# Kernel tuning notes

Hardware: AMD Instinct MI355X
Metric: run time of the kernel (lower is better)

The kernel has to match this reference:

```python
import jax, jax.numpy as jnp
import numpy as np
from jax import lax

B, S, H, T = 64, 512, 1024, 21


def setup_inputs() -> dict:
    key = jax.random.key(0)
    k1, k2, k3, k4, k5, k6, k7 = jax.random.split(key, 7)
    hidden_states = jax.random.normal(k1, (B, S, H), dtype=jnp.float32)
    attention_mask = jnp.ones((B, S), dtype=jnp.int32)
    labels = jax.random.randint(k2, (B, S), 0, T).astype(jnp.int64)
    W = jax.random.normal(k3, (T, H), dtype=jnp.float32) * 0.02
    b = jnp.zeros((T,), dtype=jnp.float32)
    # torchcrf init: uniform(-0.1, 0.1)
    transitions = jax.random.uniform(k4, (T, T), minval=-0.1, maxval=0.1, dtype=jnp.float32)
    start_transitions = jax.random.uniform(k5, (T,), minval=-0.1, maxval=0.1, dtype=jnp.float32)
    end_transitions = jax.random.uniform(k6, (T,), minval=-0.1, maxval=0.1, dtype=jnp.float32)
    return {
        "hidden_states": hidden_states,
        "attention_mask": attention_mask,
        "labels": labels,
        "W": W,
        "b": b,
        "transitions": transitions,
        "start_transitions": start_transitions,
        "end_transitions": end_transitions,
    }


def _crf_log_likelihood(emissions, labels, mask, trans, start, end):
    # emissions [B,S,T], labels [B,S] int, mask [B,S] bool. reduction='sum'.
    Bn, Sn, Tn = emissions.shape
    maskf = mask.astype(emissions.dtype)
    emit_scores = jnp.take_along_axis(emissions, labels[:, :, None], axis=2)[:, :, 0]  # [B,S]
    trans_scores = trans[labels[:, :-1], labels[:, 1:]]  # [B,S-1]
    numerator = start[labels[:, 0]] + emit_scores[:, 0]
    numerator = numerator + jnp.sum((trans_scores + emit_scores[:, 1:]) * maskf[:, 1:], axis=1)
    seq_ends = jnp.sum(mask.astype(jnp.int32), axis=1) - 1  # [B]
    last_tags = labels[jnp.arange(Bn), seq_ends]
    numerator = numerator + end[last_tags]
    # partition via forward algorithm (scan over time)
    alpha0 = start[None, :] + emissions[:, 0]  # [B,T]
    def step(alpha, inp):
        emit_t, mask_t = inp  # [B,T], [B]
        nxt = jax.nn.logsumexp(alpha[:, :, None] + trans[None, :, :] + emit_t[:, None, :], axis=1)
        return jnp.where(mask_t[:, None], nxt, alpha), None
    alpha, _ = lax.scan(step, alpha0, (emissions[:, 1:].transpose(1, 0, 2), mask[:, 1:].T))
    log_Z = jax.nn.logsumexp(alpha + end[None, :], axis=1)  # [B]
    return jnp.sum(numerator - log_Z)


def _viterbi_decode(emissions, mask, trans, start, end):
    Bn, Sn, Tn = emissions.shape
    score0 = start[None, :] + emissions[:, 0]  # [B,T]
    identity_bp = jnp.broadcast_to(jnp.arange(Tn)[None, :], (Bn, Tn))
    def fwd(score, inp):
        emit_t, mask_t = inp
        broad = score[:, :, None] + trans[None, :, :]  # [B, prev, cur]
        best_prev = jnp.argmax(broad, axis=1)  # [B,T]
        nxt = jnp.max(broad, axis=1) + emit_t
        new_score = jnp.where(mask_t[:, None], nxt, score)
        bp = jnp.where(mask_t[:, None], best_prev, identity_bp)
        return new_score, bp
    final_score, bps = lax.scan(fwd, score0, (emissions[:, 1:].transpose(1, 0, 2), mask[:, 1:].T))
    last_tag = jnp.argmax(final_score + end[None, :], axis=1)  # [B] tag at pos S-1
    def back(tag, bp_t):
        prev = jnp.take_along_axis(bp_t, tag[:, None], axis=1)[:, 0]
        return prev, tag
    tag0, tags_rest = lax.scan(back, last_tag, bps, reverse=True)  # tags_rest[t] = tag at pos t+1
    tags = jnp.concatenate([tag0[None, :], tags_rest], axis=0).T  # [B,S]
    return jnp.where(mask, tags, 0).astype(jnp.int64)


def reference(hidden_states, attention_mask, labels, W, b, transitions, start_transitions, end_transitions):
    mask = attention_mask.astype(bool)
    # dropout is identity in eval mode
    emissions = jnp.einsum("bsh,th->bst", hidden_states, W) + b  # [B,S,T]
    log_prob = _crf_log_likelihood(emissions, labels, mask, transitions, start_transitions, end_transitions)
    loss = -log_prob
    pred = _viterbi_decode(emissions, mask, transitions, start_transitions, end_transitions)
    return loss, pred
```

## Files before the change

kernel.cpp:

```cpp
#include <hip/hip_runtime.h>
#include <math.h>
#include <stdint.h>

#define BB 64
#define SS 512
#define HH 1024
#define TT 21

template <int CTRL>
__device__ __forceinline__ float dpp_add(float v) {
  int t = __builtin_amdgcn_update_dpp(0, __float_as_int(v), CTRL, 0xF, 0xF, true);
  return v + __int_as_float(t);
}
__device__ __forceinline__ float wave_sum(float v) {
  v = dpp_add<0x121>(v);
  v = dpp_add<0x122>(v);
  v = dpp_add<0x124>(v);
  v = dpp_add<0x128>(v);
  v += __shfl_xor(v, 16);
  v += __shfl_xor(v, 32);
  return v;
}

#define DOT4(A, H, WV)    \
  A = fmaf(H.x, WV.x, A); \
  A = fmaf(H.y, WV.y, A); \
  A = fmaf(H.z, WV.z, A); \
  A = fmaf(H.w, WV.w, A)

__global__ __launch_bounds__(192, 4) void k_emis(const float* __restrict__ hs,
                                                 const float* __restrict__ W,
                                                 const float* __restrict__ bias,
                                                 float* __restrict__ emis) {
  __shared__ float part[192 * 14];
  const int tid = threadIdx.x;
  const int q = tid & 7;
  const int tmp = tid >> 3;
  const int tg = tmp % 3;
  const int rp = tmp / 3;
  const size_t row0 = (size_t)blockIdx.x * 16 + rp * 2;
  const float4* hp0 = (const float4*)(hs + row0 * HH);
  const float4* hp1 = (const float4*)(hs + (row0 + 1) * HH);
  const float* wb0 = W + (size_t)(tg * 7) * HH + q * 4;

  float a0[7] = {0.f, 0.f, 0.f, 0.f, 0.f, 0.f, 0.f};
  float a1[7] = {0.f, 0.f, 0.f, 0.f, 0.f, 0.f, 0.f};
  float4 h0 = hp0[q], h1 = hp1[q];
#pragma unroll 2
  for (int i = 0; i < 32; ++i) {
    const float4 hc0 = h0, hc1 = h1;
    if (i < 31) {
      h0 = hp0[(i + 1) * 8 + q];
      h1 = hp1[(i + 1) * 8 + q];
    }
    const float* wb = wb0 + (size_t)i * 32;
#pragma unroll
    for (int lt = 0; lt < 7; ++lt) {
      const float4 w = *(const float4*)(wb + (size_t)lt * HH);
      DOT4(a0[lt], hc0, w);
      DOT4(a1[lt], hc1, w);
    }
  }
#pragma unroll
  for (int lt = 0; lt < 7; ++lt) {
    part[tid * 14 + lt] = a0[lt];
    part[tid * 14 + 7 + lt] = a1[lt];
  }
  __syncthreads();

  for (int o = tid; o < 16 * TT; o += 192) {
    const int rr = o / TT;
    const int t = o - rr * TT;
    const int tg2 = t / 7;
    const int lt2 = t - tg2 * 7;
    const float* pp = part + (((rr >> 1) * 3 + tg2) * 8) * 14 + (rr & 1) * 7 + lt2;
    float s = ((pp[0] + pp[14]) + (pp[28] + pp[42])) +
              ((pp[56] + pp[70]) + (pp[84] + pp[98]));
    emis[(size_t)blockIdx.x * (16 * TT) + o] = s + bias[t];
  }
}

#define RLF(V, K) __int_as_float(__builtin_amdgcn_readlane(__float_as_int(V), K))

__global__ __launch_bounds__(64, 1) void k_scan2(const float* __restrict__ emis,
                                                 const int* __restrict__ mask,
                                                 const int* __restrict__ labels,
                                                 const float* __restrict__ trans,
                                                 const float* __restrict__ sv,
                                                 const float* __restrict__ ev,
                                                 float* __restrict__ outv,
                                                 float* __restrict__ pred,
                                                 unsigned* __restrict__ done) {
  __shared__ float sE[SS * TT];
  __shared__ unsigned long long mb[9];
  __shared__ unsigned char bp[SS][32];
  __shared__ unsigned char sTag[SS];
  const int lane = threadIdx.x;

  if (blockIdx.x >= 128) {
    float a = 1.0001f, b2 = 0.9999f, c = 0.5f, d = 1.5f;
    for (int it = 0; it < 2048; ++it) {
#pragma unroll 128
      for (int k = 0; k < 128; ++k) {
        a = fmaf(a, 1.000001f, 1e-7f);
        b2 = fmaf(b2, 0.999999f, 2e-7f);
        c = fmaf(c, 1.000002f, 3e-7f);
        d = fmaf(d, 0.999998f, 4e-7f);
      }
      if (__hip_atomic_load(done, __ATOMIC_RELAXED, __HIP_MEMORY_SCOPE_AGENT) >= 128u)
        break;
    }
    asm volatile("" ::"v"(a), "v"(b2), "v"(c), "v"(d));
    return;
  }

  const int j = lane;
  const bool act = (j < TT);
  const int jj = act ? j : 0;
  const int b = blockIdx.x & 63;

  {
    const float4* src = (const float4*)(emis + (size_t)b * SS * TT);
    float4* dst = (float4*)sE;
    for (int i = lane; i < SS * TT / 4; i += 64) dst[i] = src[i];
#pragma unroll
    for (int w = 0; w < 8; ++w) {
      unsigned long long bm = __ballot(mask[b * SS + w * 64 + lane] != 0);
      if (lane == 0) mb[w] = bm;
    }
    if (lane == 0) mb[8] = 0ull;
  }
  __syncthreads();

  if (blockIdx.x < 64) {
    float E[TT];
#pragma unroll
    for (int i = 0; i < TT; ++i) E[i] = __expf(trans[i * TT + jj]);
    float v = act ? __expf(sv[jj] + sE[jj]) : 0.f;
    float C = 0.f;
    float nxtv[8];
#pragma unroll
    for (int k = 0; k < 8; ++k) nxtv[k] = sE[(1 + k) * TT + jj];

#define CRF_STEP(P, SHB)                                                      \
  {                                                                           \
    const int mk = (int)((swin >> ((SHB) + (P))) & 1ull);                     \
    const float ge_t = ge[P];                                                 \
    const float v0 = RLF(v, 0), v1 = RLF(v, 1), v2 = RLF(v, 2);               \
    const float v3 = RLF(v, 3), v4 = RLF(v, 4), v5 = RLF(v, 5);               \
    const float v6 = RLF(v, 6), v7 = RLF(v, 7), v8 = RLF(v, 8);               \
    const float v9 = RLF(v, 9), v10 = RLF(v, 10), v11 = RLF(v, 11);           \
    const float v12 = RLF(v, 12), v13 = RLF(v, 13), v14 = RLF(v, 14);         \
    const float v15 = RLF(v, 15), v16 = RLF(v, 16), v17 = RLF(v, 17);         \
    const float v18 = RLF(v, 18), v19 = RLF(v, 19), v20 = RLF(v, 20);         \
    float scale = 1.0f;                                                       \
    if ((P) == 7) {                                                           \
      float m = fmaxf(fmaxf(fmaxf(v0, v1), fmaxf(v2, v3)),                    \
                      fmaxf(fmaxf(v4, v5), fmaxf(v6, v7)));                   \
      m = fmaxf(m, fmaxf(fmaxf(v8, v9), fmaxf(v10, v11)));                    \
      m = fmaxf(m, fmaxf(fmaxf(v12, v13), fmaxf(v14, v15)));                  \
      m = fmaxf(m, fmaxf(fmaxf(v16, v17), fmaxf(v18, v19)));                  \
      m = fmaxf(m, v20);                                                      \
      int ex = (int)((__float_as_uint(m) >> 23) & 255u) - 127;                \
      scale = __uint_as_float((unsigned)(127 - ex) << 23);                    \
      C += (float)ex * 0.6931471805599453f;                                   \
      v *= scale;                                                             \
    }                                                                         \
    float q0 = v0 * E[0], q1 = v1 * E[1], q2 = v2 * E[2];                     \
    q0 = fmaf(v3, E[3], q0);   q1 = fmaf(v4, E[4], q1);   q2 = fmaf(v5, E[5], q2);   \
    q0 = fmaf(v6, E[6], q0);   q1 = fmaf(v7, E[7], q1);   q2 = fmaf(v8, E[8], q2);   \
    q0 = fmaf(v9, E[9], q0);   q1 = fmaf(v10, E[10], q1); q2 = fmaf(v11, E[11], q2); \
    q0 = fmaf(v12, E[12], q0); q1 = fmaf(v13, E[13], q1); q2 = fmaf(v14, E[14], q2); \
    q0 = fmaf(v15, E[15], q0); q1 = fmaf(v16, E[16], q1); q2 = fmaf(v17, E[17], q2); \
    q0 = fmaf(v18, E[18], q0); q1 = fmaf(v19, E[19], q1); q2 = fmaf(v20, E[20], q2); \
    float vn = ((q0 + q1 + q2) * scale) * ge_t;                               \
    v = (act && mk) ? vn : v;                                                 \
  }

#pragma unroll 1
    for (int w = 0; w < 8; ++w) {
      const unsigned long long wa = mb[w], wb2 = mb[w + 1];
      const unsigned long long winv = (wa >> 1) | (wb2 << 63);
      const unsigned wlo = __builtin_amdgcn_readfirstlane((unsigned)winv);
      const unsigned whi = __builtin_amdgcn_readfirstlane((unsigned)(winv >> 32));
      const unsigned long long swin = ((unsigned long long)whi << 32) | wlo;
      const int nci = (w < 7) ? 8 : 7;
#pragma unroll 1
      for (int ci = 0; ci < nci; ++ci) {
        const int t0 = ((w << 3) + ci) * 8 + 1;
        float cur[8], ge[8];
#pragma unroll
        for (int k = 0; k < 8; ++k) cur[k] = nxtv[k];
#pragma unroll
        for (int k = 0; k < 8; ++k) ge[k] = __expf(cur[k]);
#pragma unroll
        for (int k = 0; k < 8; ++k) {
          int tl = t0 + 8 + k;
          tl = (tl < SS) ? tl : (SS - 1);
          nxtv[k] = sE[tl * TT + jj];
        }
        const int shb = ci << 3;
#pragma unroll
        for (int p = 0; p < 8; ++p) { CRF_STEP(p, shb); }
      }
      if (w == 7) {
        float cur[8], ge[8];
#pragma unroll
        for (int k = 0; k < 7; ++k) cur[k] = nxtv[k];
#pragma unroll
        for (int k = 0; k < 7; ++k) ge[k] = __expf(cur[k]);
#pragma unroll
        for (int p = 0; p < 7; ++p) { CRF_STEP(p, 56); }
      }
    }
#undef CRF_STEP
    float wv = act ? v * __expf(ev[jj]) : 0.f;
#pragma unroll
    for (int d = 32; d >= 1; d >>= 1) wv += __shfl_xor(wv, d);
    const float logZv = C + __logf(wv);

    int cnt = 0;
#pragma unroll
    for (int w = 0; w < 8; ++w) cnt += (int)__popcll(mb[w]);
    const int* lab = labels + b * SS;
    float p = 0.f;
    for (int t = lane; t < SS; t += 64) {
      if (t >= 1) {
        const int lp = lab[t - 1];
        const int lc = lab[t];
        const float mk = (float)((mb[t >> 6] >> (t & 63)) & 1ull);
        p += mk * (trans[lp * TT + lc] + sE[t * TT + lc]);
      }
    }
    p = wave_sum(p);
    if (lane == 0) {
      const int l0 = lab[0];
      float numer = p + sv[l0] + sE[l0];
      numer += ev[lab[cnt - 1]];
      atomicAdd(outv, logZv - numer);
      atomicAdd(done, 1u);
    }
  } else {
    float Tc[TT];
#pragma unroll
    for (int i = 0; i < TT; ++i) Tc[i] = trans[i * TT + jj];
    float sc = act ? (sv[jj] + sE[jj]) : -3.0e38f;
    float nxtv[8];
#pragma unroll
    for (int k = 0; k < 8; ++k) nxtv[k] = sE[(1 + k) * TT + jj];

#define ARGSTEP(BV, BI, VAL, IDX)          \
  {                                        \
    float x_ = (VAL) + Tc[IDX];            \
    if (x_ > BV) { BV = x_; BI = (IDX); }  \
  }
#define VIT_STEP(P, SHB, TCUR)                                                \
  {                                                                           \
    const int mk = (int)((swin >> ((SHB) + (P))) & 1ull);                     \
    const float e = cur[P];                                                   \
    const float s0 = RLF(sc, 0), s1 = RLF(sc, 1), s2 = RLF(sc, 2);            \
    const float s3 = RLF(sc, 3), s4 = RLF(sc, 4), s5 = RLF(sc, 5);            \
    const float s6 = RLF(sc, 6), s7 = RLF(sc, 7), s8 = RLF(sc, 8);            \
    const float s9 = RLF(sc, 9), s10 = RLF(sc, 10), s11 = RLF(sc, 11);        \
    const float s12 = RLF(sc, 12), s13 = RLF(sc, 13), s14 = RLF(sc, 14);      \
    const float s15 = RLF(sc, 15), s16 = RLF(sc, 16), s17 = RLF(sc, 17);      \
    const float s18 = RLF(sc, 18), s19 = RLF(sc, 19), s20 = RLF(sc, 20);      \
    float b0v, b1v, b2v;                                                      \
    int i0, i1, i2;                                                           \
    b0v = s0 + Tc[0]; i0 = 0;                                                 \
    b1v = s1 + Tc[1]; i1 = 1;                                                 \
    b2v = s2 + Tc[2]; i2 = 2;                                                 \
    ARGSTEP(b0v, i0, s3, 3);   ARGSTEP(b1v, i1, s4, 4);   ARGSTEP(b2v, i2, s5, 5);    \
    ARGSTEP(b0v, i0, s6, 6);   ARGSTEP(b1v, i1, s7, 7);   ARGSTEP(b2v, i2, s8, 8);    \
    ARGSTEP(b0v, i0, s9, 9);   ARGSTEP(b1v, i1, s10, 10); ARGSTEP(b2v, i2, s11, 11);  \
    ARGSTEP(b0v, i0, s12, 12); ARGSTEP(b1v, i1, s13, 13); ARGSTEP(b2v, i2, s14, 14);  \
    ARGSTEP(b0v, i0, s15, 15); ARGSTEP(b1v, i1, s16, 16); ARGSTEP(b2v, i2, s17, 17);  \
    ARGSTEP(b0v, i0, s18, 18); ARGSTEP(b1v, i1, s19, 19); ARGSTEP(b2v, i2, s20, 20);  \
    float best = b0v;                                                         \
    int bi = i0;                                                              \
    if (b1v > best || (b1v == best && i1 < bi)) { best = b1v; bi = i1; }      \
    if (b2v > best || (b2v == best && i2 < bi)) { best = b2v; bi = i2; }      \
    float ns = best + e;                                                      \
    sc = (act && mk) ? ns : sc;                                               \
    if (act) bp[TCUR][j] = (unsigned char)(mk ? bi : j);                      \
  }

#pragma unroll 1
    for (int w = 0; w < 8; ++w) {
      const unsigned long long wa = mb[w], wb2 = mb[w + 1];
      const unsigned long long winv = (wa >> 1) | (wb2 << 63);
      const unsigned wlo = __builtin_amdgcn_readfirstlane((unsigned)winv);
      const unsigned whi = __builtin_amdgcn_readfirstlane((unsigned)(winv >> 32));
      const unsigned long long swin = ((unsigned long long)whi << 32) | wlo;
      const int nci = (w < 7) ? 8 : 7;
#pragma unroll 1
      for (int ci = 0; ci < nci; ++ci) {
        const int t0 = ((w << 3) + ci) * 8 + 1;
        float cur[8];
#pragma unroll
        for (int k = 0; k < 8; ++k) cur[k] = nxtv[k];
#pragma unroll
        for (int k = 0; k < 8; ++k) {
          int tl = t0 + 8 + k;
          tl = (tl < SS) ? tl : (SS - 1);
          nxtv[k] = sE[tl * TT + jj];
        }
        const int shb = ci << 3;
#pragma unroll
        for (int p = 0; p < 8; ++p) { VIT_STEP(p, shb, t0 + p); }
      }
      if (w == 7) {
        float cur[8];
#pragma unroll
        for (int k = 0; k < 7; ++k) cur[k] = nxtv[k];
#pragma unroll
        for (int p = 0; p < 7; ++p) { VIT_STEP(p, 56, 505 + p); }
      }
    }
#undef VIT_STEP
#undef ARGSTEP
    float fsv = act ? (sc + ev[jj]) : -3.0e38f;
    int idx = j;
#pragma unroll
    for (int d = 32; d >= 1; d >>= 1) {
      float ov = __shfl_xor(fsv, d);
      int oi = __shfl_xor(idx, d);
      bool take = (ov > fsv) || (ov == fsv && oi < idx);
      fsv = take ? ov : fsv;
      idx = take ? oi : idx;
    }
    __syncthreads();
    if (lane == 0) {
      int tag = idx;
      sTag[SS - 1] = (unsigned char)tag;
      for (int t = SS - 1; t >= 1; --t) {
        tag = bp[t][tag];
        sTag[t - 1] = (unsigned char)tag;
      }
    }
    __syncthreads();
    for (int i = lane; i < SS; i += 64) {
      pred[(size_t)b * SS + i] = (float)(mask[b * SS + i] ? (int)sTag[i] : 0);
    }
    if (lane == 0) atomicAdd(done, 1u);
  }
}

extern "C" void kernel_launch(void* const* d_in, const int* in_sizes, int n_in,
                              void* d_out, int out_size, void* d_ws, size_t ws_size,
                              hipStream_t stream) {
  const float* hs = (const float*)d_in[0];
  const int* msk = (const int*)d_in[1];
  const int* lab = (const int*)d_in[2];
  const float* W = (const float*)d_in[3];
  const float* bias = (const float*)d_in[4];
  const float* trans = (const float*)d_in[5];
  const float* sv = (const float*)d_in[6];
  const float* ev = (const float*)d_in[7];
  float* out = (float*)d_out;

  float* emis = (float*)d_ws;
  unsigned* done = (unsigned*)((char*)d_ws + (size_t)BB * SS * TT * 4);

  hipMemsetAsync(d_out, 0, 4, stream);
  hipMemsetAsync(done, 0, 4, stream);
  k_emis<<<2048, 192, 0, stream>>>(hs, W, bias, emis);
  k_scan2<<<512, 64, 0, stream>>>(emis, msk, lab, trans, sv, ev, out, out + 1, done);
}
```

Measured before the change: 450.5 us.

## Fuse emission GEMM into per-batch CRF/Viterbi block with pipelined producer waves

Result: slower. 1.792 ms (+297.7%).

```diff
diff --git a/kernel.cpp b/kernel.cpp
--- a/kernel.cpp
+++ b/kernel.cpp
@@ -28,131 +28,53 @@
   A = fmaf(H.z, WV.z, A); \
   A = fmaf(H.w, WV.w, A)
 
-__global__ __launch_bounds__(192, 4) void k_emis(const float* __restrict__ hs,
-                                                 const float* __restrict__ W,
-                                                 const float* __restrict__ bias,
-                                                 float* __restrict__ emis) {
-  __shared__ float part[192 * 14];
-  const int tid = threadIdx.x;
-  const int q = tid & 7;
-  const int tmp = tid >> 3;
-  const int tg = tmp % 3;
-  const int rp = tmp / 3;
-  const size_t row0 = (size_t)blockIdx.x * 16 + rp * 2;
-  const float4* hp0 = (const float4*)(hs + row0 * HH);
-  const float4* hp1 = (const float4*)(hs + (row0 + 1) * HH);
-  const float* wb0 = W + (size_t)(tg * 7) * HH + q * 4;
-
-  float a0[7] = {0.f, 0.f, 0.f, 0.f, 0.f, 0.f, 0.f};
-  float a1[7] = {0.f, 0.f, 0.f, 0.f, 0.f, 0.f, 0.f};
-  float4 h0 = hp0[q], h1 = hp1[q];
-#pragma unroll 2
-  for (int i = 0; i < 32; ++i) {
-    const float4 hc0 = h0, hc1 = h1;
-    if (i < 31) {
-      h0 = hp0[(i + 1) * 8 + q];
-      h1 = hp1[(i + 1) * 8 + q];
-    }
-    const float* wb = wb0 + (size_t)i * 32;
-#pragma unroll
-    for (int lt = 0; lt < 7; ++lt) {
-      const float4 w = *(const float4*)(wb + (size_t)lt * HH);
-      DOT4(a0[lt], hc0, w);
-      DOT4(a1[lt], hc1, w);
-    }
-  }
-#pragma unroll
-  for (int lt = 0; lt < 7; ++lt) {
-    part[tid * 14 + lt] = a0[lt];
-    part[tid * 14 + 7 + lt] = a1[lt];
-  }
-  __syncthreads();
-
-  for (int o = tid; o < 16 * TT; o += 192) {
-    const int rr = o / TT;
-    const int t = o - rr * TT;
-    const int tg2 = t / 7;
-    const int lt2 = t - tg2 * 7;
-    const float* pp = part + (((rr >> 1) * 3 + tg2) * 8) * 14 + (rr & 1) * 7 + lt2;
-    float s = ((pp[0] + pp[14]) + (pp[28] + pp[42])) +
-              ((pp[56] + pp[70]) + (pp[84] + pp[98]));
-    emis[(size_t)blockIdx.x * (16 * TT) + o] = s + bias[t];
-  }
-}
-
 #define RLF(V, K) __int_as_float(__builtin_amdgcn_readlane(__float_as_int(V), K))
 
-__global__ __launch_bounds__(64, 1) void k_scan2(const float* __restrict__ emis,
-                                                 const int* __restrict__ mask,
-                                                 const int* __restrict__ labels,
-                                                 const float* __restrict__ trans,
-                                                 const float* __restrict__ sv,
-                                                 const float* __restrict__ ev,
-                                                 float* __restrict__ outv,
-                                                 float* __restrict__ pred,
-                                                 unsigned* __restrict__ done) {
+__global__ __launch_bounds__(512) void k_fused(const float* __restrict__ hs,
+                                               const int* __restrict__ mask,
+                                               const int* __restrict__ labels,
+                                               const float* __restrict__ W,
+                                               const float* __restrict__ bias,
+                                               const float* __restrict__ trans,
+                                               const float* __restrict__ sv,
+                                               const float* __restrict__ ev,
+                                               float* __restrict__ outv,
+                                               float* __restrict__ pred) {
   __shared__ float sE[SS * TT];
   __shared__ unsigned long long mb[9];
   __shared__ unsigned char bp[SS][32];
   __shared__ unsigned char sTag[SS];
-  const int lane = threadIdx.x;
-
-  if (blockIdx.x >= 128) {
-    float a = 1.0001f, b2 = 0.9999f, c = 0.5f, d = 1.5f;
-    for (int it = 0; it < 2048; ++it) {
-#pragma unroll 128
-      for (int k = 0; k < 128; ++k) {
-        a = fmaf(a, 1.000001f, 1e-7f);
-        b2 = fmaf(b2, 0.999999f, 2e-7f);
-        c = fmaf(c, 1.000002f, 3e-7f);
-        d = fmaf(d, 0.999998f, 4e-7f);
-      }
-      if (__hip_atomic_load(done, __ATOMIC_RELAXED, __HIP_MEMORY_SCOPE_AGENT) >= 128u)
-        break;
-    }
-    asm volatile("" ::"v"(a), "v"(b2), "v"(c), "v"(d));
-    return;
-  }
-
-  const int j = lane;
-  const bool act = (j < TT);
-  const int jj = act ? j : 0;
-  const int b = blockIdx.x & 63;
-
-  {
-    const float4* src = (const float4*)(emis + (size_t)b * SS * TT);
-    float4* dst = (float4*)sE;
-    for (int i = lane; i < SS * TT / 4; i += 64) dst[i] = src[i];
+  const int tid = threadIdx.x;
+  const int wid = tid >> 6;
+  const int ln = tid & 63;
+  const int b = blockIdx.x;
+  const bool act = (ln < TT);
+  const int jj = act ? ln : 0;
+
+  if (wid == 0) {
 #pragma unroll
     for (int w = 0; w < 8; ++w) {
-      unsigned long long bm = __ballot(mask[b * SS + w * 64 + lane] != 0);
-      if (lane == 0) mb[w] = bm;
-    }
-    if (lane == 0) mb[8] = 0ull;
-  }
-  __syncthreads();
-
-  if (blockIdx.x < 64) {
-    float E[TT];
-#pragma unroll
-    for (int i = 0; i < TT; ++i) E[i] = __expf(trans[i * TT + jj]);
-    float v = act ? __expf(sv[jj] + sE[jj]) : 0.f;
-    float C = 0.f;
-    float nxtv[8];
-#pragma unroll
-    for (int k = 0; k < 8; ++k) nxtv[k] = sE[(1 + k) * TT + jj];
-
-#define CRF_STEP(P, SHB)                                                      \
+      unsigned long long bm = __ballot(mask[b * SS + w * 64 + ln] != 0);
+      if (ln == 0) mb[w] = bm;
+    }
+    if (ln == 0) mb[8] = 0ull;
+  }
+
+  float TV[TT];
+  float st = 0.f, C = 0.f;
+  float nxtv[8];
+
+#define CRF_STEP(P)                                                           \
   {                                                                           \
-    const int mk = (int)((swin >> ((SHB) + (P))) & 1ull);                     \
+    const int mk = (int)((swin >> (shb + (P))) & 1ull);                       \
     const float ge_t = ge[P];                                                 \
-    const float v0 = RLF(v, 0), v1 = RLF(v, 1), v2 = RLF(v, 2);               \
-    const float v3 = RLF(v, 3), v4 = RLF(v, 4), v5 = RLF(v, 5);               \
-    const float v6 = RLF(v, 6), v7 = RLF(v, 7), v8 = RLF(v, 8);               \
-    const float v9 = RLF(v, 9), v10 = RLF(v, 10), v11 = RLF(v, 11);           \
-    const float v12 = RLF(v, 12), v13 = RLF(v, 13), v14 = RLF(v, 14);         \
-    const float v15 = RLF(v, 15), v16 = RLF(v, 16), v17 = RLF(v, 17);         \
-    const float v18 = RLF(v, 18), v19 = RLF(v, 19), v20 = RLF(v, 20);         \
+    const float v0 = RLF(st, 0), v1 = RLF(st, 1), v2 = RLF(st, 2);            \
+    const float v3 = RLF(st, 3), v4 = RLF(st, 4), v5 = RLF(st, 5);            \
+    const float v6 = RLF(st, 6), v7 = RLF(st, 7), v8 = RLF(st, 8);            \
+    const float v9 = RLF(st, 9), v10 = RLF(st, 10), v11 = RLF(st, 11);        \
+    const float v12 = RLF(st, 12), v13 = RLF(st, 13), v14 = RLF(st, 14);      \
+    const float v15 = RLF(st, 15), v16 = RLF(st, 16), v17 = RLF(st, 17);      \
+    const float v18 = RLF(st, 18), v19 = RLF(st, 19), v20 = RLF(st, 20);      \
     float scale = 1.0f;                                                       \
     if ((P) == 7) {                                                           \
       float m = fmaxf(fmaxf(fmaxf(v0, v1), fmaxf(v2, v3)),                    \
@@ -164,112 +86,40 @@
       int ex = (int)((__float_as_uint(m) >> 23) & 255u) - 127;                \
       scale = __uint_as_float((unsigned)(127 - ex) << 23);                    \
       C += (float)ex * 0.6931471805599453f;                                   \
-      v *= scale;                                                             \
+      st *= scale;                                                            \
     }                                                                         \
-    float q0 = v0 * E[0], q1 = v1 * E[1], q2 = v2 * E[2];                     \
-    q0 = fmaf(v3, E[3], q0);   q1 = fmaf(v4, E[4], q1);   q2 = fmaf(v5, E[5], q2);   \
-    q0 = fmaf(v6, E[6], q0);   q1 = fmaf(v7, E[7], q1);   q2 = fmaf(v8, E[8], q2);   \
-    q0 = fmaf(v9, E[9], q0);   q1 = fmaf(v10, E[10], q1); q2 = fmaf(v11, E[11], q2); \
-    q0 = fmaf(v12, E[12], q0); q1 = fmaf(v13, E[13], q1); q2 = fmaf(v14, E[14], q2); \
-    q0 = fmaf(v15, E[15], q0); q1 = fmaf(v16, E[16], q1); q2 = fmaf(v17, E[17], q2); \
-    q0 = fmaf(v18, E[18], q0); q1 = fmaf(v19, E[19], q1); q2 = fmaf(v20, E[20], q2); \
+    float q0 = v0 * TV[0], q1 = v1 * TV[1], q2 = v2 * TV[2];                  \
+    q0 = fmaf(v3, TV[3], q0);   q1 = fmaf(v4, TV[4], q1);   q2 = fmaf(v5, TV[5], q2);   \
+    q0 = fmaf(v6, TV[6], q0);   q1 = fmaf(v7, TV[7], q1);   q2 = fmaf(v8, TV[8], q2);   \
+    q0 = fmaf(v9, TV[9], q0);   q1 = fmaf(v10, TV[10], q1); q2 = fmaf(v11, TV[11], q2); \
+    q0 = fmaf(v12, TV[12], q0); q1 = fmaf(v13, TV[13], q1); q2 = fmaf(v14, TV[14], q2); \
+    q0 = fmaf(v15, TV[15], q0); q1 = fmaf(v16, TV[16], q1); q2 = fmaf(v17, TV[17], q2); \
+    q0 = fmaf(v18, TV[18], q0); q1 = fmaf(v19, TV[19], q1); q2 = fmaf(v20, TV[20], q2); \
     float vn = ((q0 + q1 + q2) * scale) * ge_t;                               \
-    v = (act && mk) ? vn : v;                                                 \
-  }
-
-#pragma unroll 1
-    for (int w = 0; w < 8; ++w) {
-      const unsigned long long wa = mb[w], wb2 = mb[w + 1];
-      const unsigned long long winv = (wa >> 1) | (wb2 << 63);
-      const unsigned wlo = __builtin_amdgcn_readfirstlane((unsigned)winv);
-      const unsigned whi = __builtin_amdgcn_readfirstlane((unsigned)(winv >> 32));
-      const unsigned long long swin = ((unsigned long long)whi << 32) | wlo;
-      const int nci = (w < 7) ? 8 : 7;
-#pragma unroll 1
-      for (int ci = 0; ci < nci; ++ci) {
-        const int t0 = ((w << 3) + ci) * 8 + 1;
-        float cur[8], ge[8];
-#pragma unroll
-        for (int k = 0; k < 8; ++k) cur[k] = nxtv[k];
-#pragma unroll
-        for (int k = 0; k < 8; ++k) ge[k] = __expf(cur[k]);
-#pragma unroll
-        for (int k = 0; k < 8; ++k) {
-          int tl = t0 + 8 + k;
-          tl = (tl < SS) ? tl : (SS - 1);
-          nxtv[k] = sE[tl * TT + jj];
-        }
-        const int shb = ci << 3;
-#pragma unroll
-        for (int p = 0; p < 8; ++p) { CRF_STEP(p, shb); }
-      }
-      if (w == 7) {
-        float cur[8], ge[8];
-#pragma unroll
-        for (int k = 0; k < 7; ++k) cur[k] = nxtv[k];
-#pragma unroll
-        for (int k = 0; k < 7; ++k) ge[k] = __expf(cur[k]);
-#pragma unroll
-        for (int p = 0; p < 7; ++p) { CRF_STEP(p, 56); }
-      }
-    }
-#undef CRF_STEP
-    float wv = act ? v * __expf(ev[jj]) : 0.f;
-#pragma unroll
-    for (int d = 32; d >= 1; d >>= 1) wv += __shfl_xor(wv, d);
-    const float logZv = C + __logf(wv);
-
-    int cnt = 0;
-#pragma unroll
-    for (int w = 0; w < 8; ++w) cnt += (int)__popcll(mb[w]);
-    const int* lab = labels + b * SS;
-    float p = 0.f;
-    for (int t = lane; t < SS; t += 64) {
-      if (t >= 1) {
-        const int lp = lab[t - 1];
-        const int lc = lab[t];
-        const float mk = (float)((mb[t >> 6] >> (t & 63)) & 1ull);
-        p += mk * (trans[lp * TT + lc] + sE[t * TT + lc]);
-      }
-    }
-    p = wave_sum(p);
-    if (lane == 0) {
-      const int l0 = lab[0];
-      float numer = p + sv[l0] + sE[l0];
-      numer += ev[lab[cnt - 1]];
-      atomicAdd(outv, logZv - numer);
-      atomicAdd(done, 1u);
-    }
-  } else {
-    float Tc[TT];
-#pragma unroll
-    for (int i = 0; i < TT; ++i) Tc[i] = trans[i * TT + jj];
-    float sc = act ? (sv[jj] + sE[jj]) : -3.0e38f;
-    float nxtv[8];
-#pragma unroll
-    for (int k = 0; k < 8; ++k) nxtv[k] = sE[(1 + k) * TT + jj];
+    st = (act && mk) ? vn : st;                                               \
+  }
 
 #define ARGSTEP(BV, BI, VAL, IDX)          \
   {                                        \
-    float x_ = (VAL) + Tc[IDX];            \
+    float x_ = (VAL) + TV[IDX];            \
     if (x_ > BV) { BV = x_; BI = (IDX); }  \
   }
-#define VIT_STEP(P, SHB, TCUR)                                                \
+#define VIT_STEP(P)                                                           \
   {                                                                           \
-    const int mk = (int)((swin >> ((SHB) + (P))) & 1ull);                     \
+    const int mk = (int)((swin >> (shb + (P))) & 1ull);                       \
     const float e = cur[P];                                                   \
-    const float s0 = RLF(sc, 0), s1 = RLF(sc, 1), s2 = RLF(sc, 2);            \
-    const float s3 = RLF(sc, 3), s4 = RLF(sc, 4), s5 = RLF(sc, 5);            \
-    const float s6 = RLF(sc, 6), s7 = RLF(sc, 7), s8 = RLF(sc, 8);            \
-    const float s9 = RLF(sc, 9), s10 = RLF(sc, 10), s11 = RLF(sc, 11);        \
-    const float s12 = RLF(sc, 12), s13 = RLF(sc, 13), s14 = RLF(sc, 14);      \
-    const float s15 = RLF(sc, 15), s16 = RLF(sc, 16), s17 = RLF(sc, 17);      \
-    const float s18 = RLF(sc, 18), s19 = RLF(sc, 19), s20 = RLF(sc, 20);      \
+    const float s0 = RLF(st, 0), s1 = RLF(st, 1), s2 = RLF(st, 2);            \
+    const float s3 = RLF(st, 3), s4 = RLF(st, 4), s5 = RLF(st, 5);            \
+    const float s6 = RLF(st, 6), s7 = RLF(st, 7), s8 = RLF(st, 8);            \
+    const float s9 = RLF(st, 9), s10 = RLF(st, 10), s11 = RLF(st, 11);        \
+    const float s12 = RLF(st, 12), s13 = RLF(st, 13), s14 = RLF(st, 14);      \
+    const float s15 = RLF(st, 15), s16 = RLF(st, 16), s17 = RLF(st, 17);      \
+    const float s18 = RLF(st, 18), s19 = RLF(st, 19), s20 = RLF(st, 20);      \
     float b0v, b1v, b2v;                                                      \
     int i0, i1, i2;                                                           \
-    b0v = s0 + Tc[0]; i0 = 0;                                                 \
-    b1v = s1 + Tc[1]; i1 = 1;                                                 \
-    b2v = s2 + Tc[2]; i2 = 2;                                                 \
+    b0v = s0 + TV[0]; i0 = 0;                                                 \
+    b1v = s1 + TV[1]; i1 = 1;                                                 \
+    b2v = s2 + TV[2]; i2 = 2;                                                 \
     ARGSTEP(b0v, i0, s3, 3);   ARGSTEP(b1v, i1, s4, 4);   ARGSTEP(b2v, i2, s5, 5);    \
     ARGSTEP(b0v, i0, s6, 6);   ARGSTEP(b1v, i1, s7, 7);   ARGSTEP(b2v, i2, s8, 8);    \
     ARGSTEP(b0v, i0, s9, 9);   ARGSTEP(b1v, i1, s10, 10); ARGSTEP(b2v, i2, s11, 11);  \
@@ -281,46 +131,138 @@
     if (b1v > best || (b1v == best && i1 < bi)) { best = b1v; bi = i1; }      \
     if (b2v > best || (b2v == best && i2 < bi)) { best = b2v; bi = i2; }      \
     float ns = best + e;                                                      \
-    sc = (act && mk) ? ns : sc;                                               \
-    if (act) bp[TCUR][j] = (unsigned char)(mk ? bi : j);                      \
+    st = (act && mk) ? ns : st;                                               \
+    if (act) bp[t0 + (P)][ln] = (unsigned char)(mk ? bi : ln);                \
   }
 
 #pragma unroll 1
-    for (int w = 0; w < 8; ++w) {
-      const unsigned long long wa = mb[w], wb2 = mb[w + 1];
-      const unsigned long long winv = (wa >> 1) | (wb2 << 63);
-      const unsigned wlo = __builtin_amdgcn_readfirstlane((unsigned)winv);
-      const unsigned whi = __builtin_amdgcn_readfirstlane((unsigned)(winv >> 32));
-      const unsigned long long swin = ((unsigned long long)whi << 32) | wlo;
-      const int nci = (w < 7) ? 8 : 7;
+  for (int it = 0; it < 34; ++it) {
+    if (wid >= 2) {
+      const int p = tid - 128;
+      if (it <= 31 && p < 336) {
+        const int r = p / 21;
+        const int tg = p - r * 21;
+        const int row = it * 16 + r;
+        const float4* hp = (const float4*)(hs + ((size_t)b * SS + row) * HH);
+        const float4* wp = (const float4*)(W + (size_t)tg * HH);
+        float a[8] = {0.f, 0.f, 0.f, 0.f, 0.f, 0.f, 0.f, 0.f};
+#pragma unroll 2
+        for (int i = 0; i < 32; ++i) {
+#pragma unroll
+          for (int q = 0; q < 8; ++q) {
+            const float4 h4 = hp[i * 8 + q];
+            const float4 w4 = wp[i * 8 + q];
+            DOT4(a[q], h4, w4);
+          }
+        }
+        float s = ((a[0] + a[1]) + (a[2] + a[3])) + ((a[4] + a[5]) + (a[6] + a[7]));
+        sE[row * TT + tg] = s + bias[tg];
+      }
+    } else if (wid == 0) {
+      if (it == 2) {
+#pragma unroll
+        for (int i2 = 0; i2 < TT; ++i2) TV[i2] = __expf(trans[i2 * TT + jj]);
+        st = act ? __expf(sv[jj] + sE[jj]) : 0.f;
+        C = 0.f;
+#pragma unroll
+        for (int k = 0; k < 8; ++k) nxtv[k] = sE[(1 + k) * TT + jj];
+      }
+      if (it >= 2) {
 #pragma unroll 1
-      for (int ci = 0; ci < nci; ++ci) {
-        const int t0 = ((w << 3) + ci) * 8 + 1;
-        float cur[8];
-#pragma unroll
-        for (int k = 0; k < 8; ++k) cur[k] = nxtv[k];
-#pragma unroll
-        for (int k = 0; k < 8; ++k) {
-          int tl = t0 + 8 + k;
-          tl = (tl < SS) ? tl : (SS - 1);
-          nxtv[k] = sE[tl * TT + jj];
+        for (int u = 0; u < 2; ++u) {
+          const int s = 2 * it - 4 + u;
+          const int w = s >> 3;
+          const unsigned long long wa = mb[w], wb2 = mb[w + 1];
+          const unsigned long long winv = (wa >> 1) | (wb2 << 63);
+          const unsigned wlo = __builtin_amdgcn_readfirstlane((unsigned)winv);
+          const unsigned whi = __builtin_amdgcn_readfirstlane((unsigned)(winv >> 32));
+          const unsigned long long swin = ((unsigned long long)whi << 32) | wlo;
+          const int shb = (s & 7) << 3;
+          const int t0 = s * 8 + 1;
+          float cur[8], ge[8];
+#pragma unroll
+          for (int k = 0; k < 8; ++k) cur[k] = nxtv[k];
+#pragma unroll
+          for (int k = 0; k < 8; ++k) ge[k] = __expf(cur[k]);
+#pragma unroll
+          for (int k = 0; k < 8; ++k) {
+            int tl = t0 + 8 + k;
+            tl = (tl < SS) ? tl : (SS - 1);
+            nxtv[k] = sE[tl * TT + jj];
+          }
+#pragma unroll
+          for (int p = 0; p < 7; ++p) { CRF_STEP(p); }
+          if (s < 63) { CRF_STEP(7); }
         }
-        const int shb = ci << 3;
-#pragma unroll
-        for (int p = 0; p < 8; ++p) { VIT_STEP(p, shb, t0 + p); }
-      }
-      if (w == 7) {
-        float cur[8];
-#pragma unroll
-        for (int k = 0; k < 7; ++k) cur[k] = nxtv[k];
-#pragma unroll
-        for (int p = 0; p < 7; ++p) { VIT_STEP(p, 56, 505 + p); }
-      }
-    }
-#undef VIT_STEP
-#undef ARGSTEP
-    float fsv = act ? (sc + ev[jj]) : -3.0e38f;
-    int idx = j;
+      }
+    } else if (wid == 1) {
+      if (it == 2) {
+#pragma unroll
+        for (int i2 = 0; i2 < TT; ++i2) TV[i2] = trans[i2 * TT + jj];
+        st = act ? (sv[jj] + sE[jj]) : -3.0e38f;
+#pragma unroll
+        for (int k = 0; k < 8; ++k) nxtv[k] = sE[(1 + k) * TT + jj];
+      }
+      if (it >= 2) {
+#pragma unroll 1
+        for (int u = 0; u < 2; ++u) {
+          const int s = 2 * it - 4 + u;
+          const int w = s >> 3;
+          const unsigned long long wa = mb[w], wb2 = mb[w + 1];
+          const unsigned long long winv = (wa >> 1) | (wb2 << 63);
+          const unsigned wlo = __builtin_amdgcn_readfirstlane((unsigned)winv);
+          const unsigned whi = __builtin_amdgcn_readfirstlane((unsigned)(winv >> 32));
+          const unsigned long long swin = ((unsigned long long)whi << 32) | wlo;
+          const int shb = (s & 7) << 3;
+          const int t0 = s * 8 + 1;
+          float cur[8];
+#pragma unroll
+          for (int k = 0; k < 8; ++k) cur[k] = nxtv[k];
+#pragma unroll
+          for (int k = 0; k < 8; ++k) {
+            int tl = t0 + 8 + k;
+            tl = (tl < SS) ? tl : (SS - 1);
+            nxtv[k] = sE[tl * TT + jj];
+          }
+#pragma unroll
+          for (int p = 0; p < 7; ++p) { VIT_STEP(p); }
+          if (s < 63) { VIT_STEP(7); }
+        }
+      }
+    }
+    __syncthreads();
+  }
+
+  if (wid == 0) {
+    float wv = act ? st * __expf(ev[jj]) : 0.f;
+#pragma unroll
+    for (int d = 32; d >= 1; d >>= 1) wv += __shfl_xor(wv, d);
+    const float logZv = C + __logf(wv);
+    int cnt = 0;
+#pragma unroll
+    for (int w = 0; w < 8; ++w) cnt += (int)__popcll(mb[w]);
+    const int* lab = labels + b * SS;
+    float p = 0.f;
+    for (int t = ln; t < SS; t += 64) {
+      if (t >= 1) {
+        const int lp = lab[t - 1];
+        const int lc = lab[t];
+        const float mk = (float)((mb[t >> 6] >> (t & 63)) & 1ull);
+        p += mk * (trans[lp * TT + lc] + sE[t * TT + lc]);
+      }
+    }
+    p = wave_sum(p);
+    if (ln == 0) {
+      const int l0 = lab[0];
+      float numer = p + sv[l0] + sE[l0];
+      numer += ev[lab[cnt - 1]];
+      atomicAdd(outv, logZv - numer);
+    }
+  }
+
+  if (wid == 1) {
+    float fsv = act ? (st + ev[jj]) : -3.0e38f;
+    int idx = ln;
 #pragma unroll
     for (int d = 32; d >= 1; d >>= 1) {
       float ov = __shfl_xor(fsv, d);
@@ -329,20 +271,21 @@
       fsv = take ? ov : fsv;
       idx = take ? oi : idx;
     }
-    __syncthreads();
-    if (lane == 0) {
-      int tag = idx;
-      sTag[SS - 1] = (unsigned char)tag;
-      for (int t = SS - 1; t >= 1; --t) {
-        tag = bp[t][tag];
-        sTag[t - 1] = (unsigned char)tag;
-      }
-    }
-    __syncthreads();
-    for (int i = lane; i < SS; i += 64) {
+    if (ln == 0) sTag[SS - 1] = (unsigned char)idx;
+  }
+  __syncthreads();
+  if (wid == 1 && ln == 0) {
+    int tag = (int)sTag[SS - 1];
+    for (int t = SS - 1; t >= 1; --t) {
+      tag = bp[t][tag];
+      sTag[t - 1] = (unsigned char)tag;
+    }
+  }
+  __syncthreads();
+  if (wid == 1) {
+    for (int i = ln; i < SS; i += 64) {
       pred[(size_t)b * SS + i] = (float)(mask[b * SS + i] ? (int)sTag[i] : 0);
     }
-    if (lane == 0) atomicAdd(done, 1u);
   }
 }
 
@@ -359,11 +302,6 @@
   const float* ev = (const float*)d_in[7];
   float* out = (float*)d_out;
 
-  float* emis = (float*)d_ws;
-  unsigned* done = (unsigned*)((char*)d_ws + (size_t)BB * SS * TT * 4);
-
   hipMemsetAsync(d_out, 0, 4, stream);
-  hipMemsetAsync(done, 0, 4, stream);
-  k_emis<<<2048, 192, 0, stream>>>(hs, W, bias, emis);
-  k_scan2<<<512, 64, 0, stream>>>(emis, msk, lab, trans, sv, ev, out, out + 1, done);
+  k_fused<<<64, 512, 0, stream>>>(hs, msk, lab, W, bias, trans, sv, ev, out, out + 1);
 }
```

## Fuse emission GEMM into scan kernel, computing emissions per batch in-block

Applied to the files above, without the earlier changes.

Result: slower. 727.6 us (+61.5%).

```diff
diff --git a/kernel.cpp b/kernel.cpp
--- a/kernel.cpp
+++ b/kernel.cpp
@@ -28,119 +28,72 @@
   A = fmaf(H.z, WV.z, A); \
   A = fmaf(H.w, WV.w, A)
 
-__global__ __launch_bounds__(192, 4) void k_emis(const float* __restrict__ hs,
-                                                 const float* __restrict__ W,
-                                                 const float* __restrict__ bias,
-                                                 float* __restrict__ emis) {
-  __shared__ float part[192 * 14];
-  const int tid = threadIdx.x;
-  const int q = tid & 7;
-  const int tmp = tid >> 3;
-  const int tg = tmp % 3;
-  const int rp = tmp / 3;
-  const size_t row0 = (size_t)blockIdx.x * 16 + rp * 2;
-  const float4* hp0 = (const float4*)(hs + row0 * HH);
-  const float4* hp1 = (const float4*)(hs + (row0 + 1) * HH);
-  const float* wb0 = W + (size_t)(tg * 7) * HH + q * 4;
-
-  float a0[7] = {0.f, 0.f, 0.f, 0.f, 0.f, 0.f, 0.f};
-  float a1[7] = {0.f, 0.f, 0.f, 0.f, 0.f, 0.f, 0.f};
-  float4 h0 = hp0[q], h1 = hp1[q];
-#pragma unroll 2
-  for (int i = 0; i < 32; ++i) {
-    const float4 hc0 = h0, hc1 = h1;
-    if (i < 31) {
-      h0 = hp0[(i + 1) * 8 + q];
-      h1 = hp1[(i + 1) * 8 + q];
-    }
-    const float* wb = wb0 + (size_t)i * 32;
-#pragma unroll
-    for (int lt = 0; lt < 7; ++lt) {
-      const float4 w = *(const float4*)(wb + (size_t)lt * HH);
-      DOT4(a0[lt], hc0, w);
-      DOT4(a1[lt], hc1, w);
-    }
-  }
-#pragma unroll
-  for (int lt = 0; lt < 7; ++lt) {
-    part[tid * 14 + lt] = a0[lt];
-    part[tid * 14 + 7 + lt] = a1[lt];
-  }
-  __syncthreads();
-
-  for (int o = tid; o < 16 * TT; o += 192) {
-    const int rr = o / TT;
-    const int t = o - rr * TT;
-    const int tg2 = t / 7;
-    const int lt2 = t - tg2 * 7;
-    const float* pp = part + (((rr >> 1) * 3 + tg2) * 8) * 14 + (rr & 1) * 7 + lt2;
-    float s = ((pp[0] + pp[14]) + (pp[28] + pp[42])) +
-              ((pp[56] + pp[70]) + (pp[84] + pp[98]));
-    emis[(size_t)blockIdx.x * (16 * TT) + o] = s + bias[t];
-  }
-}
-
 #define RLF(V, K) __int_as_float(__builtin_amdgcn_readlane(__float_as_int(V), K))
 
-__global__ __launch_bounds__(64, 1) void k_scan2(const float* __restrict__ emis,
-                                                 const int* __restrict__ mask,
-                                                 const int* __restrict__ labels,
-                                                 const float* __restrict__ trans,
-                                                 const float* __restrict__ sv,
-                                                 const float* __restrict__ ev,
-                                                 float* __restrict__ outv,
-                                                 float* __restrict__ pred,
-                                                 unsigned* __restrict__ done) {
+__global__ __launch_bounds__(512) void k_all(const float* __restrict__ hs,
+                                             const int* __restrict__ mask,
+                                             const int* __restrict__ labels,
+                                             const float* __restrict__ W,
+                                             const float* __restrict__ bias,
+                                             const float* __restrict__ trans,
+                                             const float* __restrict__ sv,
+                                             const float* __restrict__ ev,
+                                             float* __restrict__ outv,
+                                             float* __restrict__ pred) {
   __shared__ float sE[SS * TT];
   __shared__ unsigned long long mb[9];
   __shared__ unsigned char bp[SS][32];
   __shared__ unsigned char sTag[SS];
-  const int lane = threadIdx.x;
-
-  if (blockIdx.x >= 128) {
-    float a = 1.0001f, b2 = 0.9999f, c = 0.5f, d = 1.5f;
-    for (int it = 0; it < 2048; ++it) {
-#pragma unroll 128
-      for (int k = 0; k < 128; ++k) {
-        a = fmaf(a, 1.000001f, 1e-7f);
-        b2 = fmaf(b2, 0.999999f, 2e-7f);
-        c = fmaf(c, 1.000002f, 3e-7f);
-        d = fmaf(d, 0.999998f, 4e-7f);
-      }
-      if (__hip_atomic_load(done, __ATOMIC_RELAXED, __HIP_MEMORY_SCOPE_AGENT) >= 128u)
-        break;
-    }
-    asm volatile("" ::"v"(a), "v"(b2), "v"(c), "v"(d));
-    return;
-  }
-
-  const int j = lane;
-  const bool act = (j < TT);
-  const int jj = act ? j : 0;
+  const int tid = threadIdx.x;
+  const int wid = tid >> 6;
+  const int ln = tid & 63;
   const int b = blockIdx.x & 63;
+  const bool isCRF = (blockIdx.x < 64);
 
   {
-    const float4* src = (const float4*)(emis + (size_t)b * SS * TT);
-    float4* dst = (float4*)sE;
-    for (int i = lane; i < SS * TT / 4; i += 64) dst[i] = src[i];
+    const int q = ln & 7;
+    const int rsub = ln >> 3;
+#pragma unroll 1
+    for (int pass = 0; pass < 8; ++pass) {
+      const int row = pass * 64 + wid * 8 + rsub;
+      const float4* hp = (const float4*)(hs + ((size_t)b * SS + row) * HH);
+      float acc[TT];
+#pragma unroll
+      for (int t = 0; t < TT; ++t) acc[t] = 0.f;
+      float4 h = hp[q];
+#pragma unroll 2
+      for (int i = 0; i < 32; ++i) {
+        const float4 hc = h;
+        if (i < 31) h = hp[(i + 1) * 8 + q];
+        const float* wb = W + i * 32 + q * 4;
+#pragma unroll
+        for (int tg = 0; tg < TT; ++tg) {
+          const float4 w4 = *(const float4*)(wb + (size_t)tg * HH);
+          DOT4(acc[tg], hc, w4);
+        }
+      }
+#pragma unroll
+      for (int tg = 0; tg < TT; ++tg) {
+        float s = acc[tg];
+        s += __shfl_xor(s, 1);
+        s += __shfl_xor(s, 2);
+        s += __shfl_xor(s, 4);
+        if (q == 0) sE[row * TT + tg] = s + bias[tg];
+      }
+    }
+  }
+  if (wid == 0) {
 #pragma unroll
     for (int w = 0; w < 8; ++w) {
-      unsigned long long bm = __ballot(mask[b * SS + w * 64 + lane] != 0);
-      if (lane == 0) mb[w] = bm;
-    }
-    if (lane == 0) mb[8] = 0ull;
+      unsigned long long bm = __ballot(mask[b * SS + w * 64 + ln] != 0);
+      if (ln == 0) mb[w] = bm;
+    }
+    if (ln == 0) mb[8] = 0ull;
   }
   __syncthreads();
 
-  if (blockIdx.x < 64) {
-    float E[TT];
-#pragma unroll
-    for (int i = 0; i < TT; ++i) E[i] = __expf(trans[i * TT + jj]);
-    float v = act ? __expf(sv[jj] + sE[jj]) : 0.f;
-    float C = 0.f;
-    float nxtv[8];
-#pragma unroll
-    for (int k = 0; k < 8; ++k) nxtv[k] = sE[(1 + k) * TT + jj];
+  const bool act = (ln < TT);
+  const int jj = act ? ln : 0;
 
 #define CRF_STEP(P, SHB)                                                      \
   {                                                                           \
@@ -177,78 +130,6 @@
     v = (act && mk) ? vn : v;                                                 \
   }
 
-#pragma unroll 1
-    for (int w = 0; w < 8; ++w) {
-      const unsigned long long wa = mb[w], wb2 = mb[w + 1];
-      const unsigned long long winv = (wa >> 1) | (wb2 << 63);
-      const unsigned wlo = __builtin_amdgcn_readfirstlane((unsigned)winv);
-      const unsigned whi = __builtin_amdgcn_readfirstlane((unsigned)(winv >> 32));
-      const unsigned long long swin = ((unsigned long long)whi << 32) | wlo;
-      const int nci = (w < 7) ? 8 : 7;
-#pragma unroll 1
-      for (int ci = 0; ci < nci; ++ci) {
-        const int t0 = ((w << 3) + ci) * 8 + 1;
-        float cur[8], ge[8];
-#pragma unroll
-        for (int k = 0; k < 8; ++k) cur[k] = nxtv[k];
-#pragma unroll
-        for (int k = 0; k < 8; ++k) ge[k] = __expf(cur[k]);
-#pragma unroll
-        for (int k = 0; k < 8; ++k) {
-          int tl = t0 + 8 + k;
-          tl = (tl < SS) ? tl : (SS - 1);
-          nxtv[k] = sE[tl * TT + jj];
-        }
-        const int shb = ci << 3;
-#pragma unroll
-        for (int p = 0; p < 8; ++p) { CRF_STEP(p, shb); }
-      }
-      if (w == 7) {
-        float cur[8], ge[8];
-#pragma unroll
-        for (int k = 0; k < 7; ++k) cur[k] = nxtv[k];
-#pragma unroll
-        for (int k = 0; k < 7; ++k) ge[k] = __expf(cur[k]);
-#pragma unroll
-        for (int p = 0; p < 7; ++p) { CRF_STEP(p, 56); }
-      }
-    }
-#undef CRF_STEP
-    float wv = act ? v * __expf(ev[jj]) : 0.f;
-#pragma unroll
-    for (int d = 32; d >= 1; d >>= 1) wv += __shfl_xor(wv, d);
-    const float logZv = C + __logf(wv);
-
-    int cnt = 0;
-#pragma unroll
-    for (int w = 0; w < 8; ++w) cnt += (int)__popcll(mb[w]);
-    const int* lab = labels + b * SS;
-    float p = 0.f;
-    for (int t = lane; t < SS; t += 64) {
-      if (t >= 1) {
-        const int lp = lab[t - 1];
-        const int lc = lab[t];
-        const float mk = (float)((mb[t >> 6] >> (t & 63)) & 1ull);
-        p += mk * (trans[lp * TT + lc] + sE[t * TT + lc]);
-      }
-    }
-    p = wave_sum(p);
-    if (lane == 0) {
-      const int l0 = lab[0];
-      float numer = p + sv[l0] + sE[l0];
-      numer += ev[lab[cnt - 1]];
-      atomicAdd(outv, logZv - numer);
-      atomicAdd(done, 1u);
-    }
-  } else {
-    float Tc[TT];
-#pragma unroll
-    for (int i = 0; i < TT; ++i) Tc[i] = trans[i * TT + jj];
-    float sc = act ? (sv[jj] + sE[jj]) : -3.0e38f;
-    float nxtv[8];
-#pragma unroll
-    for (int k = 0; k < 8; ++k) nxtv[k] = sE[(1 + k) * TT + jj];
-
 #define ARGSTEP(BV, BI, VAL, IDX)          \
   {                                        \
     float x_ = (VAL) + Tc[IDX];            \
@@ -282,8 +163,18 @@
     if (b2v > best || (b2v == best && i2 < bi)) { best = b2v; bi = i2; }      \
     float ns = best + e;                                                      \
     sc = (act && mk) ? ns : sc;                                               \
-    if (act) bp[TCUR][j] = (unsigned char)(mk ? bi : j);                      \
-  }
+    if (act) bp[TCUR][ln] = (unsigned char)(mk ? bi : ln);                    \
+  }
+
+  if (isCRF && wid == 0) {
+    float E[TT];
+#pragma unroll
+    for (int i = 0; i < TT; ++i) E[i] = __expf(trans[i * TT + jj]);
+    float v = act ? __expf(sv[jj] + sE[jj]) : 0.f;
+    float C = 0.f;
+    float nxtv[8];
+#pragma unroll
+    for (int k = 0; k < 8; ++k) nxtv[k] = sE[(1 + k) * TT + jj];
 
 #pragma unroll 1
     for (int w = 0; w < 8; ++w) {
@@ -296,9 +187,11 @@
 #pragma unroll 1
       for (int ci = 0; ci < nci; ++ci) {
         const int t0 = ((w << 3) + ci) * 8 + 1;
-        float cur[8];
+        float cur[8], ge[8];
 #pragma unroll
         for (int k = 0; k < 8; ++k) cur[k] = nxtv[k];
+#pragma unroll
+        for (int k = 0; k < 8; ++k) ge[k] = __expf(cur[k]);
 #pragma unroll
         for (int k = 0; k < 8; ++k) {
           int tl = t0 + 8 + k;
@@ -307,6 +200,74 @@
         }
         const int shb = ci << 3;
 #pragma unroll
+        for (int p = 0; p < 8; ++p) { CRF_STEP(p, shb); }
+      }
+      if (w == 7) {
+        float cur[8], ge[8];
+#pragma unroll
+        for (int k = 0; k < 7; ++k) cur[k] = nxtv[k];
+#pragma unroll
+        for (int k = 0; k < 7; ++k) ge[k] = __expf(cur[k]);
+#pragma unroll
+        for (int p = 0; p < 7; ++p) { CRF_STEP(p, 56); }
+      }
+    }
+    float wv = act ? v * __expf(ev[jj]) : 0.f;
+#pragma unroll
+    for (int d = 32; d >= 1; d >>= 1) wv += __shfl_xor(wv, d);
+    const float logZv = C + __logf(wv);
+
+    int cnt = 0;
+#pragma unroll
+    for (int w = 0; w < 8; ++w) cnt += (int)__popcll(mb[w]);
+    const int* lab = labels + b * SS;
+    float p = 0.f;
+    for (int t = ln; t < SS; t += 64) {
+      if (t >= 1) {
+        const int lp = lab[t - 1];
+        const int lc = lab[t];
+        const float mk = (float)((mb[t >> 6] >> (t & 63)) & 1ull);
+        p += mk * (trans[lp * TT + lc] + sE[t * TT + lc]);
+      }
+    }
+    p = wave_sum(p);
+    if (ln == 0) {
+      const int l0 = lab[0];
+      float numer = p + sv[l0] + sE[l0];
+      numer += ev[lab[cnt - 1]];
+      atomicAdd(outv, logZv - numer);
+    }
+  } else if (!isCRF && wid == 0) {
+    float Tc[TT];
+#pragma unroll
+    for (int i = 0; i < TT; ++i) Tc[i] = trans[i * TT + jj];
+    float sc = act ? (sv[jj] + sE[jj]) : -3.0e38f;
+    float nxtv[8];
+#pragma unroll
+    for (int k = 0; k < 8; ++k) nxtv[k] = sE[(1 + k) * TT + jj];
+
+#pragma unroll 1
+    for (int w = 0; w < 8; ++w) {
+      const unsigned long long wa = mb[w], wb2 = mb[w + 1];
+      const unsigned long long winv = (wa >> 1) | (wb2 << 63);
+      const unsigned wlo = __builtin_amdgcn_readfirstlane((unsigned)winv);
+      const unsigned whi = __builtin_amdgcn_readfirstlane((unsigned)(winv >> 32));
+      const unsigned long long swin = ((unsigned long long)whi << 32) | wlo;
+      const int nci = (w < 7) ? 8 : 7;
+#pragma unroll 1
+      for (int ci = 0; ci < nci; ++ci) {
+        const int t0 = ((w << 3) + ci) * 8 + 1;
+        float cur[8];
+#pragma unroll
+        for (int k = 0; k < 8; ++k) cur[k] = nxtv[k];
+#pragma unroll
+        for (int k = 0; k < 8; ++k) {
+          int tl = t0 + 8 + k;
+          tl = (tl < SS) ? tl : (SS - 1);
+          nxtv[k] = sE[tl * TT + jj];
+        }
+        const int shb = ci << 3;
+#pragma unroll
         for (int p = 0; p < 8; ++p) { VIT_STEP(p, shb, t0 + p); }
       }
       if (w == 7) {
@@ -317,10 +278,8 @@
         for (int p = 0; p < 7; ++p) { VIT_STEP(p, 56, 505 + p); }
       }
     }
-#undef VIT_STEP
-#undef ARGSTEP
     float fsv = act ? (sc + ev[jj]) : -3.0e38f;
-    int idx = j;
+    int idx = ln;
 #pragma unroll
     for (int d = 32; d >= 1; d >>= 1) {
       float ov = __shfl_xor(fsv, d);
@@ -329,21 +288,26 @@
       fsv = take ? ov : fsv;
       idx = take ? oi : idx;
     }
-    __syncthreads();
-    if (lane == 0) {
-      int tag = idx;
-      sTag[SS - 1] = (unsigned char)tag;
-      for (int t = SS - 1; t >= 1; --t) {
-        tag = bp[t][tag];
-        sTag[t - 1] = (unsigned char)tag;
-      }
-    }
-    __syncthreads();
-    for (int i = lane; i < SS; i += 64) {
+    if (ln == 0) sTag[SS - 1] = (unsigned char)idx;
+  }
+
+  __syncthreads();
+  if (!isCRF && wid == 0 && ln == 0) {
+    int tag = (int)sTag[SS - 1];
+    for (int t = SS - 1; t >= 1; --t) {
+      tag = bp[t][tag];
+      sTag[t - 1] = (unsigned char)tag;
+    }
+  }
+  __syncthreads();
+  if (!isCRF) {
+    for (int i = tid; i < SS; i += 512) {
       pred[(size_t)b * SS + i] = (float)(mask[b * SS + i] ? (int)sTag[i] : 0);
     }
-    if (lane == 0) atomicAdd(done, 1u);
-  }
+  }
+#undef VIT_STEP
+#undef ARGSTEP
+#undef CRF_STEP
 }
 
 extern "C" void kernel_launch(void* const* d_in, const int* in_sizes, int n_in,
@@ -359,11 +323,6 @@
   const float* ev = (const float*)d_in[7];
   float* out = (float*)d_out;
 
-  float* emis = (float*)d_ws;
-  unsigned* done = (unsigned*)((char*)d_ws + (size_t)BB * SS * TT * 4);
-
   hipMemsetAsync(d_out, 0, 4, stream);
-  hipMemsetAsync(done, 0, 4, stream);
-  k_emis<<<2048, 192, 0, stream>>>(hs, W, bias, emis);
-  k_scan2<<<512, 64, 0, stream>>>(emis, msk, lab, trans, sv, ev, out, out + 1, done);
+  k_all<<<128, 512, 0, stream>>>(hs, msk, lab, W, bias, trans, sv, ev, out, out + 1);
 }
```
